# Optimization experiments

Measured on AMD Instinct MI355X. Metric: run time of the kernel, lower is better.

The kernel has to match this reference:

```python
import jax, jax.numpy as jnp
import numpy as np

K = 50
EPS = 1e-8


def setup_inputs() -> dict:
    key = jax.random.key(0)
    k1, k2 = jax.random.split(key)
    B, S, V = 2, 2048, 50257
    p = jax.random.uniform(k1, (B, S, V), dtype=jnp.float32)
    q = jax.random.uniform(k2, (B, S, V), dtype=jnp.float32)
    # normalize to probability distributions over the vocab dim
    p = p / jnp.sum(p, axis=-1, keepdims=True)
    q = q / jnp.sum(q, axis=-1, keepdims=True)
    return {"p": p, "q": q}


def _kl(p, q):
    p_safe = p + EPS
    q_safe = q + EPS
    return jnp.sum(p_safe * jnp.log(p_safe / q_safe), axis=-1)


def reference(p, q):
    B, S, V = p.shape
    N = B * S
    p_flat = p.reshape(N, V)
    q_flat = q.reshape(N, V)

    _, p_idx = jax.lax.top_k(p_flat, K)  # [N, K]
    _, q_idx = jax.lax.top_k(q_flat, K)  # [N, K]

    rows = jnp.arange(N)[:, None]  # [N, 1]
    mask = jnp.zeros((N, V), dtype=bool)
    mask = mask.at[rows, p_idx].set(True)
    mask = mask.at[rows, q_idx].set(True)

    p_m = jnp.where(mask, p_flat, 0.0)
    q_m = jnp.where(mask, q_flat, 0.0)

    p_m = p_m / (jnp.sum(p_m, axis=-1, keepdims=True) + EPS)
    q_m = q_m / (jnp.sum(q_m, axis=-1, keepdims=True) + EPS)

    m = 0.5 * (p_m + q_m)
    jsd = 0.5 * _kl(p_m, m) + 0.5 * _kl(q_m, m)  # [N]
    return jsd.reshape(B, S)
```

## Files before the change

kernel.cpp:

```cpp
#include <hip/hip_runtime.h>
#include <stdint.h>

#define NTHREADS 256
#define KTOP 50
#define CAP 1024
#define EPSV 1e-8f

typedef unsigned long long u64;
typedef uint32_t u32;
typedef float __attribute__((ext_vector_type(4))) f4;

#define C_CNTP 0
#define C_CNTQ 1
#define C_OVF  2
#define C_GEN  3

__device__ __forceinline__ float block_max(float v, float* s_f, int tid) {
    for (int off = 32; off; off >>= 1) v = fmaxf(v, __shfl_down(v, off));
    if ((tid & 63) == 0) s_f[tid >> 6] = v;
    __syncthreads();
    if (tid == 0) {
        float m = s_f[0];
        for (int w = 1; w < NTHREADS / 64; ++w) m = fmaxf(m, s_f[w]);
        s_f[4] = m;
    }
    __syncthreads();
    float r = s_f[4];
    __syncthreads();
    return r;
}

__device__ __forceinline__ void push32(u32* cand, u32* cnt, u32* ovf,
                                       float v, int idx, float t, u32 tbits) {
    if (v >= t) {
        u32 delta = __float_as_uint(v) - tbits;
        if (delta > 0xFFFFu) { *ovf = 1u; delta = 0xFFFFu; }
        u32 pos = atomicAdd(cnt, 1u);
        if (pos < CAP) cand[pos] = (delta << 16) | (0xFFFFu - (u32)idx);
    }
}

__device__ __forceinline__ void push64(u64* cand, u32* cnt,
                                       float v, int idx, float t) {
    if (v >= t) {
        u32 pos = atomicAdd(cnt, 1u);
        if (pos < CAP)
            cand[pos] = (((u64)__float_as_uint(v)) << 16) |
                        (u64)(0xFFFFu - (u32)idx);
    }
}

__device__ int collect_direct64(const float* __restrict__ row, int V, float t,
                                u64* cand, u32* s_cnt, int tid) {
    if (tid == 0) *s_cnt = 0;
    __syncthreads();
    int mis = (int)(((uintptr_t)row >> 2) & 3);
    int head = (4 - mis) & 3; if (head > V) head = V;
    if (tid < head) push64(cand, s_cnt, row[tid], tid, t);
    int nvec = (V - head) >> 2;
    const float4* vr = reinterpret_cast<const float4*>(row + head);
    for (int i = tid; i < nvec; i += NTHREADS) {
        float4 v = vr[i];
        int b = head + (i << 2);
        push64(cand, s_cnt, v.x, b, t);     push64(cand, s_cnt, v.y, b + 1, t);
        push64(cand, s_cnt, v.z, b + 2, t); push64(cand, s_cnt, v.w, b + 3, t);
    }
    for (int i = head + (nvec << 2) + tid; i < V; i += NTHREADS)
        push64(cand, s_cnt, row[i], i, t);
    __syncthreads();
    int n = (int)*s_cnt;
    __syncthreads();
    return n;
}

__device__ void find_topk64(const u64* cand, int nc, uint16_t* top,
                            u64* s_merge, int tid) {
    int lane = tid & 63, w = tid >> 6;
    u64 r0 = 0, r1 = 0, r2 = 0, r3 = 0;
    int j0 = (w << 6) + lane;
    if (j0 < nc)       r0 = cand[j0];
    if (j0 + 256 < nc) r1 = cand[j0 + 256];
    if (j0 + 512 < nc) r2 = cand[j0 + 512];
    if (j0 + 768 < nc) r3 = cand[j0 + 768];
    for (int k = 0; k < KTOP; ++k) {
        u64 a = r0 > r1 ? r0 : r1;
        u64 b = r2 > r3 ? r2 : r3;
        u64 m = a > b ? a : b;
        #pragma unroll
        for (int off = 32; off; off >>= 1) {
            u64 o = __shfl_xor(m, off);
            if (o > m) m = o;
        }
        if (lane == 0) s_merge[w * KTOP + k] = m;
        if (r0 == m) r0 = 0; else if (r1 == m) r1 = 0;
        else if (r2 == m) r2 = 0; else if (r3 == m) r3 = 0;
    }
    __syncthreads();
    if (w == 0) {
        u64 q0 = 0, q1 = 0, q2 = 0, q3 = 0;
        if (lane < 4 * KTOP)       q0 = s_merge[lane];
        if (lane + 64 < 4 * KTOP)  q1 = s_merge[lane + 64];
        if (lane + 128 < 4 * KTOP) q2 = s_merge[lane + 128];
        if (lane + 192 < 4 * KTOP) q3 = s_merge[lane + 192];
        for (int k = 0; k < KTOP; ++k) {
            u64 a = q0 > q1 ? q0 : q1;
            u64 b = q2 > q3 ? q2 : q3;
            u64 m = a > b ? a : b;
            #pragma unroll
            for (int off = 32; off; off >>= 1) {
                u64 o = __shfl_xor(m, off);
                if (o > m) m = o;
            }
            if (lane == 0) top[k] = (uint16_t)(0xFFFFu - (u32)(m & 0xFFFFu));
            if (q0 == m) q0 = 0; else if (q1 == m) q1 = 0;
            else if (q2 == m) q2 = 0; else if (q3 == m) q3 = 0;
        }
    }
    __syncthreads();
}

template <int NR>
__device__ void find32(const u32* cand, int nc, uint16_t* top, int lane) {
    u32 r[NR];
    #pragma unroll
    for (int j = 0; j < NR; ++j) {
        int idx = lane + j * 64;
        r[j] = (idx < nc) ? cand[idx] : 0u;
    }
    u32 mine = 0;
    for (int k = 0; k < KTOP; ++k) {
        u32 m = 0;
        #pragma unroll
        for (int j = 0; j < NR; ++j) m = r[j] > m ? r[j] : m;
        #pragma unroll
        for (int off = 32; off; off >>= 1) {
            u32 o = __shfl_xor(m, off);
            m = o > m ? o : m;
        }
        if (lane == k) mine = m;
        #pragma unroll
        for (int j = 0; j < NR; ++j) if (r[j] == m) r[j] = 0;
    }
    if (lane < KTOP) top[lane] = (uint16_t)(0xFFFFu - (mine & 0xFFFFu));
}

#define ISSUE1(R, PTR) \
    asm volatile("global_load_dwordx4 %0, %1, off" \
                 : "=&v"(R) : "v"(PTR))

#define WAITV(N) do { \
    asm volatile("s_waitcnt vmcnt(" #N ")" ::: "memory"); \
    __builtin_amdgcn_sched_barrier(0); } while (0)

#define CONSUME1(R, G) do { \
    float _m = fmaxf(fmaxf(R.x, R.y), fmaxf(R.z, R.w)); \
    if (_m >= t) { \
        int _e = head + (((G) * NTHREADS + tid) << 2); \
        push32(cand, cnt, ovf, R.x, _e,     t, tbits); \
        push32(cand, cnt, ovf, R.y, _e + 1, t, tbits); \
        push32(cand, cnt, ovf, R.z, _e + 2, t, tbits); \
        push32(cand, cnt, ovf, R.w, _e + 3, t, tbits); \
    } } while (0)

__device__ __forceinline__ void stream_one(
    const float* __restrict__ row, int V, float t, u32 tbits,
    u32* cand, u32* cnt, u32* ovf, int tid)
{
    int mis = (int)(((uintptr_t)row >> 2) & 3);
    int head = (4 - mis) & 3; if (head > V) head = V;
    int nvec = (V - head) >> 2;
    const f4* v4 = reinterpret_cast<const f4*>(row + head);

    if (tid < head) push32(cand, cnt, ovf, row[tid], tid, t, tbits);

    int ngrp = nvec / NTHREADS;
    int ring = 0;
    if (ngrp >= 12) {
        f4 s0, s1, s2, s3, s4, s5;
        const f4* pp = v4 + tid;
        ISSUE1(s0, pp); pp += NTHREADS;
        ISSUE1(s1, pp); pp += NTHREADS;
        ISSUE1(s2, pp); pp += NTHREADS;
        ISSUE1(s3, pp); pp += NTHREADS;
        ISSUE1(s4, pp); pp += NTHREADS;
        ISSUE1(s5, pp); pp += NTHREADS;
        int gend6 = ((ngrp - 6) / 6) * 6;
        int g = 0;
        for (; g < gend6; g += 6) {
            WAITV(5); CONSUME1(s0, g + 0); ISSUE1(s0, pp); pp += NTHREADS;
            WAITV(5); CONSUME1(s1, g + 1); ISSUE1(s1, pp); pp += NTHREADS;
            WAITV(5); CONSUME1(s2, g + 2); ISSUE1(s2, pp); pp += NTHREADS;
            WAITV(5); CONSUME1(s3, g + 3); ISSUE1(s3, pp); pp += NTHREADS;
            WAITV(5); CONSUME1(s4, g + 4); ISSUE1(s4, pp); pp += NTHREADS;
            WAITV(5); CONSUME1(s5, g + 5); ISSUE1(s5, pp); pp += NTHREADS;
        }
        WAITV(0);
        CONSUME1(s0, g + 0);
        CONSUME1(s1, g + 1);
        CONSUME1(s2, g + 2);
        CONSUME1(s3, g + 3);
        CONSUME1(s4, g + 4);
        CONSUME1(s5, g + 5);
        ring = g + 6;
    }

    for (int i = ring * NTHREADS + tid; i < nvec; i += NTHREADS) {
        f4 a = v4[i];
        int e = head + (i << 2);
        push32(cand, cnt, ovf, a.x, e,     t, tbits);
        push32(cand, cnt, ovf, a.y, e + 1, t, tbits);
        push32(cand, cnt, ovf, a.z, e + 2, t, tbits);
        push32(cand, cnt, ovf, a.w, e + 3, t, tbits);
    }
    for (int i = head + (nvec << 2) + tid; i < V; i += NTHREADS)
        push32(cand, cnt, ovf, row[i], i, t, tbits);
}

__global__ __launch_bounds__(NTHREADS, 8)
void topk_jsd_kernel(const float* __restrict__ p, const float* __restrict__ q,
                     float* __restrict__ out, int V)
{
    __shared__ u64 candRaw[CAP];
    __shared__ u64 s_merge[4 * KTOP];
    __shared__ float s_f[8];
    __shared__ u32 s_c[4];
    __shared__ uint16_t topP[KTOP];
    __shared__ uint16_t topQ[KTOP];
    __shared__ uint16_t s_union[2 * KTOP];
    __shared__ int s_nu;

    u32* candP = (u32*)candRaw;
    u32* candQ = ((u32*)candRaw) + CAP;

    const int row = blockIdx.x;
    const int tid = threadIdx.x;
    const int lane = tid & 63, w = tid >> 6;
    const float* prow = p + (size_t)row * (size_t)V;
    const float* qrow = q + (size_t)row * (size_t)V;

    int smp = V < 2048 ? V : 2048;
    float msP = 0.f, msQ = 0.f;
    for (int i = tid; i < smp; i += NTHREADS) {
        msP = fmaxf(msP, prow[i]);
        msQ = fmaxf(msQ, qrow[i]);
    }
    float MsP = block_max(msP, s_f, tid);
    float MsQ = block_max(msQ, s_f, tid);

    float eps0 = fminf(128.f / (float)V + 1.f / (float)smp, 0.5f);
    float tP = MsP * (1.f - eps0);
    float tQ = MsQ * (1.f - eps0);
    u32 tPb = __float_as_uint(tP), tQb = __float_as_uint(tQ);

    if (tid == 0) { s_c[0] = 0; s_c[1] = 0; s_c[2] = 0; }
    __syncthreads();

    stream_one(prow, V, tP, tPb, candP, &s_c[C_CNTP], &s_c[C_OVF], tid);
    stream_one(qrow, V, tQ, tQb, candQ, &s_c[C_CNTQ], &s_c[C_OVF], tid);

    __syncthreads();
    int ncP = (int)s_c[C_CNTP];
    int ncQ = (int)s_c[C_CNTQ];
    u32 ovf = s_c[C_OVF];
    __syncthreads();

    bool okP = !ovf && ncP >= KTOP && ncP <= CAP;
    bool okQ = !ovf && ncQ >= KTOP && ncQ <= CAP;

    if (okP && w == 0) {
        if (ncP <= 256) find32<4>(candP, ncP, topP, lane);
        else            find32<16>(candP, ncP, topP, lane);
    }
    if (okQ && w == 1) {
        if (ncQ <= 256) find32<4>(candQ, ncQ, topQ, lane);
        else            find32<16>(candQ, ncQ, topQ, lane);
    }

    if (!okP) {
        float eps = eps0;
        int nc = collect_direct64(prow, V, MsP * (1.f - eps), candRaw, &s_c[C_GEN], tid);
        for (int a = 0; a < 10 && (nc < KTOP || nc > CAP); ++a) {
            eps = (nc > CAP) ? eps * 0.25f : fminf(eps * 4.f, 1.f);
            nc = collect_direct64(prow, V, MsP * (1.f - eps), candRaw, &s_c[C_GEN], tid);
        }
        if (nc > CAP) nc = CAP;
        find_topk64(candRaw, nc, topP, s_merge, tid);
    }
    if (!okQ) {
        float eps = eps0;
        int nc = collect_direct64(qrow, V, MsQ * (1.f - eps), candRaw, &s_c[C_GEN], tid);
        for (int a = 0; a < 10 && (nc < KTOP || nc > CAP); ++a) {
            eps = (nc > CAP) ? eps * 0.25f : fminf(eps * 4.f, 1.f);
            nc = collect_direct64(qrow, V, MsQ * (1.f - eps), candRaw, &s_c[C_GEN], tid);
        }
        if (nc > CAP) nc = CAP;
        find_topk64(candRaw, nc, topQ, s_merge, tid);
    }
    __syncthreads();

    if (tid < KTOP) s_union[tid] = topP[tid];
    __syncthreads();
    if (tid < 64) {
        bool freshb = false; uint16_t qi = 0;
        if (tid < KTOP) {
            qi = topQ[tid]; freshb = true;
            for (int j = 0; j < KTOP; ++j) if (topP[j] == qi) freshb = false;
        }
        u64 mb = __ballot(freshb);
        int pos = __popcll(mb & ((1ull << tid) - 1ull));
        if (freshb) s_union[KTOP + pos] = qi;
        if (tid == 0) s_nu = KTOP + __popcll(mb);
    }
    __syncthreads();
    int nu = s_nu;

    float pv = 0.f, qv = 0.f;
    if (tid < nu) {
        int ui = s_union[tid]; ui = ui < V ? ui : V - 1;
        pv = prow[ui];
        qv = qrow[ui];
    }

    float sp = pv, sq = qv;
    for (int off = 32; off; off >>= 1) { sp += __shfl_down(sp, off); sq += __shfl_down(sq, off); }
    if ((tid & 63) == 0) { s_f[w] = sp; s_f[4 + w] = sq; }
    __syncthreads();
    if (tid == 0) {
        float a = 0.f, b = 0.f;
        for (int ww = 0; ww < NTHREADS / 64; ++ww) { a += s_f[ww]; b += s_f[4 + ww]; }
        s_f[0] = a; s_f[4] = b;
    }
    __syncthreads();
    float sump = s_f[0], sumq = s_f[4];
    __syncthreads();

    float term = 0.f;
    if (tid < nu) {
        float pn = pv / (sump + EPSV);
        float qn = qv / (sumq + EPSV);
        float mn = 0.5f * (pn + qn);
        float ps = pn + EPSV, qs = qn + EPSV, ms = mn + EPSV;
        term = 0.5f * (ps * logf(ps / ms) + qs * logf(qs / ms));
    }
    for (int off = 32; off; off >>= 1) term += __shfl_down(term, off);
    if ((tid & 63) == 0) s_f[w] = term;
    __syncthreads();
    if (tid == 0) {
        float a = 0.f;
        for (int ww = 0; ww < NTHREADS / 64; ++ww) a += s_f[ww];
        out[row] = a;
    }
}

extern "C" void kernel_launch(void* const* d_in, const int* in_sizes, int n_in,
                              void* d_out, int out_size, void* d_ws, size_t ws_size,
                              hipStream_t stream) {
    const float* p = (const float*)d_in[0];
    const float* q = (const float*)d_in[1];
    float* out = (float*)d_out;
    if (out_size <= 0) return;
    int N = out_size;
    int V = in_sizes[0] / N;
    topk_jsd_kernel<<<dim3(N), dim3(NTHREADS), 0, stream>>>(p, q, out, V);
}
```

Baseline: 408.8 us.

## Split top-k JSD into threshold, segmented stream, and finish kernels

Replaces the single per-row kernel with three launches. One computes per-row thresholds, one streams each row of p and q in four segments across eight blocks per row and appends candidates to a global workspace buffer, and one selects the top-k and computes the JSD. The aim is more parallelism and memory-level concurrency for the bandwidth-bound streaming pass, since one block per row gives only 4096 blocks handling both p and q serially. The cost is extra launches, global atomics and round trips through the workspace. It falls back to the fused kernel when no workspace is available.

Result: slower. 419.2 us (+2.6%).

```diff
diff --git a/kernel.cpp b/kernel.cpp
--- a/kernel.cpp
+++ b/kernel.cpp
@@ -4,6 +4,8 @@
 #define NTHREADS 256
 #define KTOP 50
 #define CAP 1024
+#define SEGCAP 512
+#define NSEG 4
 #define EPSV 1e-8f
 
 typedef unsigned long long u64;
@@ -31,12 +33,13 @@
 }
 
 __device__ __forceinline__ void push32(u32* cand, u32* cnt, u32* ovf,
-                                       float v, int idx, float t, u32 tbits) {
+                                       float v, int idx, float t, u32 tbits,
+                                       u32 cap) {
     if (v >= t) {
         u32 delta = __float_as_uint(v) - tbits;
         if (delta > 0xFFFFu) { *ovf = 1u; delta = 0xFFFFu; }
         u32 pos = atomicAdd(cnt, 1u);
-        if (pos < CAP) cand[pos] = (delta << 16) | (0xFFFFu - (u32)idx);
+        if (pos < cap) cand[pos] = (delta << 16) | (0xFFFFu - (u32)idx);
     }
 }
 
@@ -152,32 +155,15 @@
     asm volatile("s_waitcnt vmcnt(" #N ")" ::: "memory"); \
     __builtin_amdgcn_sched_barrier(0); } while (0)
 
-#define CONSUME1(R, G) do { \
-    float _m = fmaxf(fmaxf(R.x, R.y), fmaxf(R.z, R.w)); \
-    if (_m >= t) { \
-        int _e = head + (((G) * NTHREADS + tid) << 2); \
-        push32(cand, cnt, ovf, R.x, _e,     t, tbits); \
-        push32(cand, cnt, ovf, R.y, _e + 1, t, tbits); \
-        push32(cand, cnt, ovf, R.z, _e + 2, t, tbits); \
-        push32(cand, cnt, ovf, R.w, _e + 3, t, tbits); \
-    } } while (0)
-
-__device__ __forceinline__ void stream_one(
-    const float* __restrict__ row, int V, float t, u32 tbits,
-    u32* cand, u32* cnt, u32* ovf, int tid)
-{
-    int mis = (int)(((uintptr_t)row >> 2) & 3);
-    int head = (4 - mis) & 3; if (head > V) head = V;
-    int nvec = (V - head) >> 2;
-    const f4* v4 = reinterpret_cast<const f4*>(row + head);
-
-    if (tid < head) push32(cand, cnt, ovf, row[tid], tid, t, tbits);
-
-    int ngrp = nvec / NTHREADS;
+template <typename CB>
+__device__ __forceinline__ void stream_range(const f4* __restrict__ v4,
+                                             int lo, int hi, int tid, CB&& cb) {
+    int len = hi - lo;
+    int ngrp = len / NTHREADS;
     int ring = 0;
     if (ngrp >= 12) {
         f4 s0, s1, s2, s3, s4, s5;
-        const f4* pp = v4 + tid;
+        const f4* pp = v4 + lo + tid;
         ISSUE1(s0, pp); pp += NTHREADS;
         ISSUE1(s1, pp); pp += NTHREADS;
         ISSUE1(s2, pp); pp += NTHREADS;
@@ -187,33 +173,247 @@
         int gend6 = ((ngrp - 6) / 6) * 6;
         int g = 0;
         for (; g < gend6; g += 6) {
-            WAITV(5); CONSUME1(s0, g + 0); ISSUE1(s0, pp); pp += NTHREADS;
-            WAITV(5); CONSUME1(s1, g + 1); ISSUE1(s1, pp); pp += NTHREADS;
-            WAITV(5); CONSUME1(s2, g + 2); ISSUE1(s2, pp); pp += NTHREADS;
-            WAITV(5); CONSUME1(s3, g + 3); ISSUE1(s3, pp); pp += NTHREADS;
-            WAITV(5); CONSUME1(s4, g + 4); ISSUE1(s4, pp); pp += NTHREADS;
-            WAITV(5); CONSUME1(s5, g + 5); ISSUE1(s5, pp); pp += NTHREADS;
+            WAITV(5); cb(s0, lo + (g + 0) * NTHREADS + tid); ISSUE1(s0, pp); pp += NTHREADS;
+            WAITV(5); cb(s1, lo + (g + 1) * NTHREADS + tid); ISSUE1(s1, pp); pp += NTHREADS;
+            WAITV(5); cb(s2, lo + (g + 2) * NTHREADS + tid); ISSUE1(s2, pp); pp += NTHREADS;
+            WAITV(5); cb(s3, lo + (g + 3) * NTHREADS + tid); ISSUE1(s3, pp); pp += NTHREADS;
+            WAITV(5); cb(s4, lo + (g + 4) * NTHREADS + tid); ISSUE1(s4, pp); pp += NTHREADS;
+            WAITV(5); cb(s5, lo + (g + 5) * NTHREADS + tid); ISSUE1(s5, pp); pp += NTHREADS;
         }
         WAITV(0);
-        CONSUME1(s0, g + 0);
-        CONSUME1(s1, g + 1);
-        CONSUME1(s2, g + 2);
-        CONSUME1(s3, g + 3);
-        CONSUME1(s4, g + 4);
-        CONSUME1(s5, g + 5);
+        cb(s0, lo + (g + 0) * NTHREADS + tid);
+        cb(s1, lo + (g + 1) * NTHREADS + tid);
+        cb(s2, lo + (g + 2) * NTHREADS + tid);
+        cb(s3, lo + (g + 3) * NTHREADS + tid);
+        cb(s4, lo + (g + 4) * NTHREADS + tid);
+        cb(s5, lo + (g + 5) * NTHREADS + tid);
         ring = g + 6;
     }
-
-    for (int i = ring * NTHREADS + tid; i < nvec; i += NTHREADS) {
-        f4 a = v4[i];
-        int e = head + (i << 2);
-        push32(cand, cnt, ovf, a.x, e,     t, tbits);
-        push32(cand, cnt, ovf, a.y, e + 1, t, tbits);
-        push32(cand, cnt, ovf, a.z, e + 2, t, tbits);
-        push32(cand, cnt, ovf, a.w, e + 3, t, tbits);
-    }
-    for (int i = head + (nvec << 2) + tid; i < V; i += NTHREADS)
-        push32(cand, cnt, ovf, row[i], i, t, tbits);
+    for (int i = lo + ring * NTHREADS + tid; i < hi; i += NTHREADS)
+        cb(v4[i], i);
+}
+
+__device__ void jsd_epilogue(const float* __restrict__ prow,
+                             const float* __restrict__ qrow, int V,
+                             const uint16_t* topP, const uint16_t* topQ,
+                             uint16_t* s_union, int* s_nu, float* s_f,
+                             float* __restrict__ out, int row, int tid) {
+    int w = tid >> 6;
+    if (tid < KTOP) s_union[tid] = topP[tid];
+    __syncthreads();
+    if (tid < 64) {
+        bool freshb = false; uint16_t qi = 0;
+        if (tid < KTOP) {
+            qi = topQ[tid]; freshb = true;
+            for (int j = 0; j < KTOP; ++j) if (topP[j] == qi) freshb = false;
+        }
+        u64 mb = __ballot(freshb);
+        int pos = __popcll(mb & ((1ull << tid) - 1ull));
+        if (freshb) s_union[KTOP + pos] = qi;
+        if (tid == 0) *s_nu = KTOP + __popcll(mb);
+    }
+    __syncthreads();
+    int nu = *s_nu;
+
+    float pv = 0.f, qv = 0.f;
+    if (tid < nu) {
+        int ui = s_union[tid]; ui = ui < V ? ui : V - 1;
+        pv = prow[ui];
+        qv = qrow[ui];
+    }
+    float sp = pv, sq = qv;
+    for (int off = 32; off; off >>= 1) { sp += __shfl_down(sp, off); sq += __shfl_down(sq, off); }
+    if ((tid & 63) == 0) { s_f[w] = sp; s_f[4 + w] = sq; }
+    __syncthreads();
+    if (tid == 0) {
+        float a = 0.f, b = 0.f;
+        for (int ww = 0; ww < NTHREADS / 64; ++ww) { a += s_f[ww]; b += s_f[4 + ww]; }
+        s_f[0] = a; s_f[4] = b;
+    }
+    __syncthreads();
+    float sump = s_f[0], sumq = s_f[4];
+    __syncthreads();
+
+    float term = 0.f;
+    if (tid < nu) {
+        float pn = pv / (sump + EPSV);
+        float qn = qv / (sumq + EPSV);
+        float mn = 0.5f * (pn + qn);
+        float ps = pn + EPSV, qs = qn + EPSV, ms = mn + EPSV;
+        term = 0.5f * (ps * logf(ps / ms) + qs * logf(qs / ms));
+    }
+    for (int off = 32; off; off >>= 1) term += __shfl_down(term, off);
+    if ((tid & 63) == 0) s_f[w] = term;
+    __syncthreads();
+    if (tid == 0) {
+        float a = 0.f;
+        for (int ww = 0; ww < NTHREADS / 64; ++ww) a += s_f[ww];
+        out[row] = a;
+    }
+}
+
+__global__ __launch_bounds__(NTHREADS)
+void thresh_kernel(const float* __restrict__ p, const float* __restrict__ q,
+                   u32* __restrict__ cnt, u32* __restrict__ ovfw,
+                   float* __restrict__ msarr, u32* __restrict__ tb, int V)
+{
+    __shared__ float s_f[8];
+    int row = blockIdx.x, tid = threadIdx.x;
+    const float* prow = p + (size_t)row * (size_t)V;
+    const float* qrow = q + (size_t)row * (size_t)V;
+    int smp = V < 2048 ? V : 2048;
+    float msP = 0.f, msQ = 0.f;
+    for (int i = tid; i < smp; i += NTHREADS) {
+        msP = fmaxf(msP, prow[i]);
+        msQ = fmaxf(msQ, qrow[i]);
+    }
+    float MsP = block_max(msP, s_f, tid);
+    float MsQ = block_max(msQ, s_f, tid);
+    float eps0 = fminf(128.f / (float)V + 1.f / (float)smp, 0.5f);
+    if (tid == 0) {
+        msarr[2 * row]     = MsP;
+        msarr[2 * row + 1] = MsQ;
+        tb[2 * row]     = __float_as_uint(MsP * (1.f - eps0));
+        tb[2 * row + 1] = __float_as_uint(MsQ * (1.f - eps0));
+        cnt[2 * row] = 0;  cnt[2 * row + 1] = 0;
+        ovfw[2 * row] = 0; ovfw[2 * row + 1] = 0;
+    }
+}
+
+__global__ __launch_bounds__(NTHREADS, 8)
+void stream_kernel(const float* __restrict__ p, const float* __restrict__ q,
+                   u32* __restrict__ cnt, u32* __restrict__ ovfw,
+                   const u32* __restrict__ tb, u32* __restrict__ cands, int V)
+{
+    __shared__ u32 candL[SEGCAP];
+    __shared__ u32 s_nL;
+    __shared__ u32 s_base;
+
+    int bid = blockIdx.x;
+    int row   = bid >> 3;
+    int r     = bid & 7;
+    int which = r >> 2;
+    int seg   = r & 3;
+    int tid = threadIdx.x;
+
+    const float* rw = (which ? q : p) + (size_t)row * (size_t)V;
+    int slot = 2 * row + which;
+    u32 tbits = tb[slot];
+    float t = __uint_as_float(tbits);
+    u32* gcand = cands + (size_t)slot * CAP;
+
+    if (tid == 0) s_nL = 0;
+    __syncthreads();
+
+    int mis = (int)(((uintptr_t)rw >> 2) & 3);
+    int head = (4 - mis) & 3; if (head > V) head = V;
+    int nvec = (V - head) >> 2;
+    int lo = (int)(((long long)nvec * seg) / NSEG);
+    int hi = (int)(((long long)nvec * (seg + 1)) / NSEG);
+    const f4* v4 = reinterpret_cast<const f4*>(rw + head);
+
+    auto pushL = [&](float v, int idx) {
+        if (v >= t) {
+            u32 delta = __float_as_uint(v) - tbits;
+            if (delta > 0xFFFFu) { ovfw[slot] = 1u; delta = 0xFFFFu; }
+            u32 pos = atomicAdd(&s_nL, 1u);
+            if (pos < SEGCAP) candL[pos] = (delta << 16) | (0xFFFFu - (u32)idx);
+        }
+    };
+
+    if (seg == 0 && tid < head) pushL(rw[tid], tid);
+
+    stream_range(v4, lo, hi, tid, [&](f4 v, int fi) {
+        float m = fmaxf(fmaxf(v.x, v.y), fmaxf(v.z, v.w));
+        if (m >= t) {
+            int e = head + (fi << 2);
+            pushL(v.x, e); pushL(v.y, e + 1); pushL(v.z, e + 2); pushL(v.w, e + 3);
+        }
+    });
+
+    if (seg == NSEG - 1)
+        for (int i = head + (nvec << 2) + tid; i < V; i += NTHREADS)
+            pushL(rw[i], i);
+
+    __syncthreads();
+    u32 nL = s_nL;
+    if (nL > SEGCAP) {
+        if (tid == 0) { ovfw[slot] = 1u; atomicAdd(&cnt[slot], nL); }
+        return;
+    }
+    if (tid == 0) s_base = nL ? atomicAdd(&cnt[slot], nL) : 0u;
+    __syncthreads();
+    u32 base = s_base;
+    for (u32 i = tid; i < nL; i += NTHREADS) {
+        u32 d = base + i;
+        if (d < CAP) gcand[d] = candL[i];
+    }
+}
+
+__global__ __launch_bounds__(NTHREADS)
+void finish_kernel(const float* __restrict__ p, const float* __restrict__ q,
+                   const u32* __restrict__ cnt, const u32* __restrict__ ovfw,
+                   const float* __restrict__ msarr, const u32* __restrict__ cands,
+                   float* __restrict__ out, int V)
+{
+    __shared__ u64 candRaw[CAP];
+    __shared__ u64 s_merge[4 * KTOP];
+    __shared__ float s_f[8];
+    __shared__ u32 s_c[4];
+    __shared__ uint16_t topP[KTOP];
+    __shared__ uint16_t topQ[KTOP];
+    __shared__ uint16_t s_union[2 * KTOP];
+    __shared__ int s_nu;
+
+    int row = blockIdx.x, tid = threadIdx.x;
+    int lane = tid & 63, w = tid >> 6;
+    const float* prow = p + (size_t)row * (size_t)V;
+    const float* qrow = q + (size_t)row * (size_t)V;
+
+    int ncP = (int)cnt[2 * row], ncQ = (int)cnt[2 * row + 1];
+    u32 ovP = ovfw[2 * row], ovQ = ovfw[2 * row + 1];
+    bool okP = !ovP && ncP >= KTOP && ncP <= CAP;
+    bool okQ = !ovQ && ncQ >= KTOP && ncQ <= CAP;
+
+    if (okP && w == 0) {
+        const u32* cp = cands + (size_t)(2 * row) * CAP;
+        if (ncP <= 256) find32<4>(cp, ncP, topP, lane);
+        else            find32<16>(cp, ncP, topP, lane);
+    }
+    if (okQ && w == 1) {
+        const u32* cq = cands + (size_t)(2 * row + 1) * CAP;
+        if (ncQ <= 256) find32<4>(cq, ncQ, topQ, lane);
+        else            find32<16>(cq, ncQ, topQ, lane);
+    }
+
+    int smp = V < 2048 ? V : 2048;
+    float eps0 = fminf(128.f / (float)V + 1.f / (float)smp, 0.5f);
+
+    if (!okP) {
+        float Ms = msarr[2 * row];
+        float eps = eps0;
+        int nc = collect_direct64(prow, V, Ms * (1.f - eps), candRaw, &s_c[C_GEN], tid);
+        for (int a = 0; a < 10 && (nc < KTOP || nc > CAP); ++a) {
+            eps = (nc > CAP) ? eps * 0.25f : fminf(eps * 4.f, 1.f);
+            nc = collect_direct64(prow, V, Ms * (1.f - eps), candRaw, &s_c[C_GEN], tid);
+        }
+        if (nc > CAP) nc = CAP;
+        find_topk64(candRaw, nc, topP, s_merge, tid);
+    }
+    if (!okQ) {
+        float Ms = msarr[2 * row + 1];
+        float eps = eps0;
+        int nc = collect_direct64(qrow, V, Ms * (1.f - eps), candRaw, &s_c[C_GEN], tid);
+        for (int a = 0; a < 10 && (nc < KTOP || nc > CAP); ++a) {
+            eps = (nc > CAP) ? eps * 0.25f : fminf(eps * 4.f, 1.f);
+            nc = collect_direct64(qrow, V, Ms * (1.f - eps), candRaw, &s_c[C_GEN], tid);
+        }
+        if (nc > CAP) nc = CAP;
+        find_topk64(candRaw, nc, topQ, s_merge, tid);
+    }
+    __syncthreads();
+
+    jsd_epilogue(prow, qrow, V, topP, topQ, s_union, &s_nu, s_f, out, row, tid);
 }
 
 __global__ __launch_bounds__(NTHREADS, 8)
@@ -255,8 +455,44 @@
     if (tid == 0) { s_c[0] = 0; s_c[1] = 0; s_c[2] = 0; }
     __syncthreads();
 
-    stream_one(prow, V, tP, tPb, candP, &s_c[C_CNTP], &s_c[C_OVF], tid);
-    stream_one(qrow, V, tQ, tQb, candQ, &s_c[C_CNTQ], &s_c[C_OVF], tid);
+    {
+        int mis = (int)(((uintptr_t)prow >> 2) & 3);
+        int head = (4 - mis) & 3; if (head > V) head = V;
+        int nvec = (V - head) >> 2;
+        const f4* v4 = reinterpret_cast<const f4*>(prow + head);
+        if (tid < head) push32(candP, &s_c[C_CNTP], &s_c[C_OVF], prow[tid], tid, tP, tPb, CAP);
+        stream_range(v4, 0, nvec, tid, [&](f4 v, int fi) {
+            float m = fmaxf(fmaxf(v.x, v.y), fmaxf(v.z, v.w));
+            if (m >= tP) {
+                int e = head + (fi << 2);
+                push32(candP, &s_c[C_CNTP], &s_c[C_OVF], v.x, e,     tP, tPb, CAP);
+                push32(candP, &s_c[C_CNTP], &s_c[C_OVF], v.y, e + 1, tP, tPb, CAP);
+                push32(candP, &s_c[C_CNTP], &s_c[C_OVF], v.z, e + 2, tP, tPb, CAP);
+                push32(candP, &s_c[C_CNTP], &s_c[C_OVF], v.w, e + 3, tP, tPb, CAP);
+            }
+        });
+        for (int i = head + (nvec << 2) + tid; i < V; i += NTHREADS)
+            push32(candP, &s_c[C_CNTP], &s_c[C_OVF], prow[i], i, tP, tPb, CAP);
+    }
+    {
+        int mis = (int)(((uintptr_t)qrow >> 2) & 3);
+        int head = (4 - mis) & 3; if (head > V) head = V;
+        int nvec = (V - head) >> 2;
+        const f4* v4 = reinterpret_cast<const f4*>(qrow + head);
+        if (tid < head) push32(candQ, &s_c[C_CNTQ], &s_c[C_OVF], qrow[tid], tid, tQ, tQb, CAP);
+        stream_range(v4, 0, nvec, tid, [&](f4 v, int fi) {
+            float m = fmaxf(fmaxf(v.x, v.y), fmaxf(v.z, v.w));
+            if (m >= tQ) {
+                int e = head + (fi << 2);
+                push32(candQ, &s_c[C_CNTQ], &s_c[C_OVF], v.x, e,     tQ, tQb, CAP);
+                push32(candQ, &s_c[C_CNTQ], &s_c[C_OVF], v.y, e + 1, tQ, tQb, CAP);
+                push32(candQ, &s_c[C_CNTQ], &s_c[C_OVF], v.z, e + 2, tQ, tQb, CAP);
+                push32(candQ, &s_c[C_CNTQ], &s_c[C_OVF], v.w, e + 3, tQ, tQb, CAP);
+            }
+        });
+        for (int i = head + (nvec << 2) + tid; i < V; i += NTHREADS)
+            push32(candQ, &s_c[C_CNTQ], &s_c[C_OVF], qrow[i], i, tQ, tQb, CAP);
+    }
 
     __syncthreads();
     int ncP = (int)s_c[C_CNTP];
@@ -298,58 +534,7 @@
     }
     __syncthreads();
 
-    if (tid < KTOP) s_union[tid] = topP[tid];
-    __syncthreads();
-    if (tid < 64) {
-        bool freshb = false; uint16_t qi = 0;
-        if (tid < KTOP) {
-            qi = topQ[tid]; freshb = true;
-            for (int j = 0; j < KTOP; ++j) if (topP[j] == qi) freshb = false;
-        }
-        u64 mb = __ballot(freshb);
-        int pos = __popcll(mb & ((1ull << tid) - 1ull));
-        if (freshb) s_union[KTOP + pos] = qi;
-        if (tid == 0) s_nu = KTOP + __popcll(mb);
-    }
-    __syncthreads();
-    int nu = s_nu;
-
-    float pv = 0.f, qv = 0.f;
-    if (tid < nu) {
-        int ui = s_union[tid]; ui = ui < V ? ui : V - 1;
-        pv = prow[ui];
-        qv = qrow[ui];
-    }
-
-    float sp = pv, sq = qv;
-    for (int off = 32; off; off >>= 1) { sp += __shfl_down(sp, off); sq += __shfl_down(sq, off); }
-    if ((tid & 63) == 0) { s_f[w] = sp; s_f[4 + w] = sq; }
-    __syncthreads();
-    if (tid == 0) {
-        float a = 0.f, b = 0.f;
-        for (int ww = 0; ww < NTHREADS / 64; ++ww) { a += s_f[ww]; b += s_f[4 + ww]; }
-        s_f[0] = a; s_f[4] = b;
-    }
-    __syncthreads();
-    float sump = s_f[0], sumq = s_f[4];
-    __syncthreads();
-
-    float term = 0.f;
-    if (tid < nu) {
-        float pn = pv / (sump + EPSV);
-        float qn = qv / (sumq + EPSV);
-        float mn = 0.5f * (pn + qn);
-        float ps = pn + EPSV, qs = qn + EPSV, ms = mn + EPSV;
-        term = 0.5f * (ps * logf(ps / ms) + qs * logf(qs / ms));
-    }
-    for (int off = 32; off; off >>= 1) term += __shfl_down(term, off);
-    if ((tid & 63) == 0) s_f[w] = term;
-    __syncthreads();
-    if (tid == 0) {
-        float a = 0.f;
-        for (int ww = 0; ww < NTHREADS / 64; ++ww) a += s_f[ww];
-        out[row] = a;
-    }
+    jsd_epilogue(prow, qrow, V, topP, topQ, s_union, &s_nu, s_f, out, row, tid);
 }
 
 extern "C" void kernel_launch(void* const* d_in, const int* in_sizes, int n_in,
@@ -361,5 +546,18 @@
     if (out_size <= 0) return;
     int N = out_size;
     int V = in_sizes[0] / N;
-    topk_jsd_kernel<<<dim3(N), dim3(NTHREADS), 0, stream>>>(p, q, out, V);
-}
+    size_t slots = (size_t)2 * N;
+    size_t need = slots * 4 * sizeof(u32) + slots * CAP * sizeof(u32);
+    if (d_ws && ws_size >= need && V >= 64) {
+        u32* cnt    = (u32*)d_ws;
+        u32* ovfw   = cnt + slots;
+        float* msar = (float*)(ovfw + slots);
+        u32* tb     = (u32*)(msar + slots);
+        u32* cands  = tb + slots;
+        thresh_kernel<<<dim3(N), dim3(NTHREADS), 0, stream>>>(p, q, cnt, ovfw, msar, tb, V);
+        stream_kernel<<<dim3(N * 2 * NSEG), dim3(NTHREADS), 0, stream>>>(p, q, cnt, ovfw, tb, cands, V);
+        finish_kernel<<<dim3(N), dim3(NTHREADS), 0, stream>>>(p, q, cnt, ovfw, msar, cands, out, V);
+    } else {
+        topk_jsd_kernel<<<dim3(N), dim3(NTHREADS), 0, stream>>>(p, q, out, V);
+    }
+}
```
